# Performance work log

Hardware: AMD Instinct MI355X
Metric: run time of the kernel (lower is better)

The kernel has to match this reference:

```python
import jax, jax.numpy as jnp
import numpy as np

NUM_EMB = 512
EMB_DIM = 64
COMMIT = 0.25
DECAY = 0.99
EPS = 1e-05


def setup_inputs() -> dict:
    key = jax.random.key(0)
    k1, k2, k3 = jax.random.split(key, 3)
    inputs = jax.random.normal(k1, (EMB_DIM, 16, 8192), dtype=jnp.float32)  # [D, B, T]
    embedding = jax.random.normal(k2, (NUM_EMB, EMB_DIM), dtype=jnp.float32)
    ema_w = jax.random.normal(k3, (NUM_EMB, EMB_DIM), dtype=jnp.float32)
    ema_cluster_size = jnp.zeros((NUM_EMB,), dtype=jnp.float32)
    return {"inputs": inputs, "embedding": embedding, "ema_w": ema_w,
            "ema_cluster_size": ema_cluster_size}


def reference(inputs, embedding, ema_w, ema_cluster_size):
    # [D, B, T] -> [B, T, D]
    x = jnp.transpose(inputs, (1, 2, 0))
    in_shape = x.shape
    flat = x.reshape(-1, EMB_DIM)  # [N, D]

    # Squared L2 distances to every codebook entry: [N, K]
    distances = (jnp.sum(flat ** 2, axis=1, keepdims=True)
                 + jnp.sum(embedding ** 2, axis=1)
                 - 2.0 * flat @ embedding.T)
    idx = jnp.argmin(distances, axis=1)                       # [N]
    encodings = jax.nn.one_hot(idx, NUM_EMB, dtype=jnp.float32)  # [N, K]

    # EMA codebook update (training mode). torch wraps results in nn.Parameter,
    # which detaches them, so we stop_gradient the updated embedding.
    cluster = ema_cluster_size * DECAY + (1.0 - DECAY) * jnp.sum(encodings, axis=0)
    n = jnp.sum(cluster)
    cluster = (cluster + EPS) / (n + NUM_EMB * EPS) * n
    dw = jax.ops.segment_sum(flat, idx, num_segments=NUM_EMB)  # == encodings.T @ flat
    new_ema_w = ema_w * DECAY + (1.0 - DECAY) * dw
    new_emb = jax.lax.stop_gradient(new_ema_w / cluster[:, None])  # [K, D]

    # Quantize via gather (equivalent to encodings @ new_emb)
    quantized = new_emb[idx].reshape(in_shape)  # [B, T, D]

    e_latent_loss = jnp.mean((jax.lax.stop_gradient(quantized) - x) ** 2)
    loss = COMMIT * e_latent_loss

    # Straight-through estimator
    quantized_st = x + jax.lax.stop_gradient(quantized - x)

    avg_probs = jnp.mean(encodings, axis=0)
    perplexity = jnp.exp(-jnp.sum(avg_probs * jnp.log(avg_probs + 1e-10)))

    return (loss, jnp.transpose(quantized_st, (2, 0, 1)), perplexity, encodings, distances)
```

## Files before the change

kernel.cpp:

```cpp
#include <hip/hip_runtime.h>

#define NTOT 131072
#define KCB  512
#define DIM  64

__device__ __forceinline__ float wave_sum(float v) {
#pragma unroll
  for (int off = 32; off; off >>= 1) v += __shfl_xor(v, off, 64);
  return v;
}

__global__ __launch_bounds__(512, 1) void k_prep(
    const float* __restrict__ emb, float* __restrict__ embT,
    float* __restrict__ embsq)
{
  const int k = threadIdx.x;
  float sq = 0.f;
#pragma unroll 8
  for (int d = 0; d < DIM; ++d) {
    const float e = emb[k * DIM + d];
    sq = fmaf(e, e, sq);
    embT[d * KCB + k] = -2.f * e;
  }
  embsq[k] = sq;
}

__global__ __launch_bounds__(512, 3) void k_dist(
    const float* __restrict__ x_g,
    const float* __restrict__ embT,
    const float* __restrict__ embsq,
    float* __restrict__ dist_out,
    float* __restrict__ enc_out,
    int* __restrict__ idx_out,
    unsigned* __restrict__ cnt_g,
    float* __restrict__ dw_g)
{
  __shared__ __align__(16) float xls[8][8][65];
  __shared__ unsigned lcnt[KCB];

  const int t = threadIdx.x;
  const int lane = t & 63;
  const int w = t >> 6;

  lcnt[t] = 0u;
  __syncthreads();

  const float4 eb0 = *reinterpret_cast<const float4*>(embsq + 4 * lane);
  const float4 eb1 = *reinterpret_cast<const float4*>(embsq + 256 + 4 * lane);
  float ebr[8] = {eb0.x, eb0.y, eb0.z, eb0.w, eb1.x, eb1.y, eb1.z, eb1.w};

  const int nb = blockIdx.x * 512;
  const int r_own = lane & 7;
  const int dgc   = lane >> 3;

  float xv[8];
  {
    const int n0w = nb + w * 8;
#pragma unroll
    for (int j = 0; j < 8; ++j)
      xv[j] = x_g[(size_t)(dgc * 8 + j) * NTOT + n0w + r_own];
  }

  for (int tt = 0; tt < 8; ++tt) {
    const int n0w = nb + tt * 64 + w * 8;

    asm volatile("" ::: "memory");

#pragma unroll
    for (int j = 0; j < 8; ++j)
      xls[w][r_own][dgc * 8 + j] = xv[j];

    asm volatile("" ::: "memory");

    float ps = 0.f;
#pragma unroll
    for (int j = 0; j < 8; ++j) ps = fmaf(xv[j], xv[j], ps);
    ps += __shfl_xor(ps, 8, 64);
    ps += __shfl_xor(ps, 16, 64);
    ps += __shfl_xor(ps, 32, 64);

    float xr[8];
#pragma unroll
    for (int r = 0; r < 8; ++r) xr[r] = xls[w][r][lane];

    float acc[8][8];
#pragma unroll
    for (int r = 0; r < 8; ++r)
#pragma unroll
      for (int j = 0; j < 8; ++j) acc[r][j] = ebr[j];

#pragma unroll 2
    for (int d = 0; d < DIM; ++d) {
      const float* er = embT + d * KCB + 4 * lane;
      const float4 e0 = *reinterpret_cast<const float4*>(er);
      const float4 e1 = *reinterpret_cast<const float4*>(er + 256);
#pragma unroll
      for (int r = 0; r < 8; ++r) {
        const float s = __uint_as_float(
            __builtin_amdgcn_readlane(__float_as_uint(xr[r]), d));
        acc[r][0] = fmaf(s, e0.x, acc[r][0]);
        acc[r][1] = fmaf(s, e0.y, acc[r][1]);
        acc[r][2] = fmaf(s, e0.z, acc[r][2]);
        acc[r][3] = fmaf(s, e0.w, acc[r][3]);
        acc[r][4] = fmaf(s, e1.x, acc[r][4]);
        acc[r][5] = fmaf(s, e1.y, acc[r][5]);
        acc[r][6] = fmaf(s, e1.z, acc[r][6]);
        acc[r][7] = fmaf(s, e1.w, acc[r][7]);
      }
    }

    if (tt < 7) {
      const int n1w = nb + (tt + 1) * 64 + w * 8;
#pragma unroll
      for (int j = 0; j < 8; ++j)
        xv[j] = x_g[(size_t)(dgc * 8 + j) * NTOT + n1w + r_own];
    }
    asm volatile("" ::: "memory");

#pragma unroll
    for (int r = 0; r < 8; ++r) {
      const int nr = n0w + r;
      const float xs = __uint_as_float(
          __builtin_amdgcn_readlane(__float_as_uint(ps), r));
      float dv[8];
#pragma unroll
      for (int j = 0; j < 8; ++j) dv[j] = acc[r][j] + xs;

      unsigned long long best = ~0ull;
#pragma unroll
      for (int j = 0; j < 8; ++j) {
        const unsigned kk = (j < 4) ? (unsigned)(4 * lane + j)
                                    : (unsigned)(256 + 4 * lane + (j - 4));
        const unsigned long long pk =
            ((unsigned long long)__float_as_uint(dv[j]) << 32) | kk;
        best = pk < best ? pk : best;
      }
#pragma unroll
      for (int off = 32; off; off >>= 1) {
        const unsigned long long o = __shfl_xor(best, off, 64);
        best = o < best ? o : best;
      }
      const int kmin = (int)(best & 0xFFFFFFFFull);

      float* dp = dist_out + (size_t)nr * KCB + 4 * lane;
      float4 q;
      q.x = dv[0]; q.y = dv[1]; q.z = dv[2]; q.w = dv[3];
      *reinterpret_cast<float4*>(dp) = q;
      q.x = dv[4]; q.y = dv[5]; q.z = dv[6]; q.w = dv[7];
      *reinterpret_cast<float4*>(dp + 256) = q;

      float* ep = enc_out + (size_t)nr * KCB + 4 * lane;
      const int k0 = 4 * lane;
      float4 z;
      z.x = (kmin == k0)     ? 1.f : 0.f;
      z.y = (kmin == k0 + 1) ? 1.f : 0.f;
      z.z = (kmin == k0 + 2) ? 1.f : 0.f;
      z.w = (kmin == k0 + 3) ? 1.f : 0.f;
      *reinterpret_cast<float4*>(ep) = z;
      z.x = (kmin == 256 + k0)     ? 1.f : 0.f;
      z.y = (kmin == 256 + k0 + 1) ? 1.f : 0.f;
      z.z = (kmin == 256 + k0 + 2) ? 1.f : 0.f;
      z.w = (kmin == 256 + k0 + 3) ? 1.f : 0.f;
      *reinterpret_cast<float4*>(ep + 256) = z;

      if (lane == 0) {
        idx_out[nr] = kmin;
        atomicAdd(&lcnt[kmin], 1u);
      }
      unsafeAtomicAdd(dw_g + ((size_t)kmin << 6) + lane, xr[r]);
    }
  }

  __syncthreads();
  if (lcnt[t]) atomicAdd(&cnt_g[t], lcnt[t]);
}

__global__ __launch_bounds__(512, 1) void k_final(
    const float* __restrict__ ema_w, const float* __restrict__ ema_cs,
    const unsigned* __restrict__ cnt, const float* __restrict__ dw,
    float* __restrict__ nemb, float* __restrict__ out)
{
  __shared__ float red[8];
  __shared__ float bc;
  const int t = threadIdx.x;
  const int lane = t & 63, w = t >> 6;

  const float c = (float)cnt[t];
  const float craw = ema_cs[t] * 0.99f + 0.01f * c;

  float s = wave_sum(craw);
  if (lane == 0) red[w] = s;
  __syncthreads();
  if (t == 0) {
    float a = 0.f;
#pragma unroll
    for (int i = 0; i < 8; ++i) a += red[i];
    bc = a;
  }
  __syncthreads();
  const float n = bc;
  const float clus = (craw + 1e-5f) / (n + 512.f * 1e-5f) * n;

  const float4* wr = reinterpret_cast<const float4*>(ema_w + t * 64);
  const float4* dr = reinterpret_cast<const float4*>(dw + t * 64);
  float4* nr = reinterpret_cast<float4*>(nemb + t * 64);
#pragma unroll
  for (int q = 0; q < 16; ++q) {
    const float4 wv = wr[q], dv = dr[q];
    float4 o;
    o.x = (wv.x * 0.99f + 0.01f * dv.x) / clus;
    o.y = (wv.y * 0.99f + 0.01f * dv.y) / clus;
    o.z = (wv.z * 0.99f + 0.01f * dv.z) / clus;
    o.w = (wv.w * 0.99f + 0.01f * dv.w) / clus;
    nr[q] = o;
  }

  const float p = c * (1.f / 131072.f);
  const float term = p * logf(p + 1e-10f);
  float s2 = wave_sum(term);
  if (lane == 0) red[w] = s2;
  __syncthreads();
  if (t == 0) {
    float a = 0.f;
#pragma unroll
    for (int i = 0; i < 8; ++i) a += red[i];
    out[8388609] = expf(-a);
  }
}

__global__ __launch_bounds__(256, 4) void k_quant(
    const float* __restrict__ x_g, const int* __restrict__ idx_g,
    const float* __restrict__ nemb, float* __restrict__ out)
{
  float lsum = 0.f;
  const int stride = gridDim.x * 256;
  for (int i = blockIdx.x * 256 + threadIdx.x; i < (DIM * NTOT / 4); i += stride) {
    const int d = i >> 15;
    const int n4 = i & ((NTOT / 4) - 1);
    const float4 xv = *reinterpret_cast<const float4*>(x_g + ((size_t)d << 17) + 4 * n4);
    const int4 id = *reinterpret_cast<const int4*>(idx_g + 4 * n4);
    const float q0 = nemb[(id.x << 6) + d];
    const float q1 = nemb[(id.y << 6) + d];
    const float q2 = nemb[(id.z << 6) + d];
    const float q3 = nemb[(id.w << 6) + d];
    const float e0 = q0 - xv.x, e1 = q1 - xv.y, e2 = q2 - xv.z, e3 = q3 - xv.w;
    float* op = out + 1 + ((size_t)d << 17) + 4 * n4;
    op[0] = xv.x + e0;
    op[1] = xv.y + e1;
    op[2] = xv.z + e2;
    op[3] = xv.w + e3;
    lsum += e0 * e0 + e1 * e1 + e2 * e2 + e3 * e3;
  }
  lsum = wave_sum(lsum);
  __shared__ float wsum[4];
  const int lane = threadIdx.x & 63, w = threadIdx.x >> 6;
  if (lane == 0) wsum[w] = lsum;
  __syncthreads();
  if (threadIdx.x == 0)
    unsafeAtomicAdd(out, (wsum[0] + wsum[1] + wsum[2] + wsum[3]) * (0.25f / 8388608.f));
}

extern "C" void kernel_launch(void* const* d_in, const int* in_sizes, int n_in,
                              void* d_out, int out_size, void* d_ws, size_t ws_size,
                              hipStream_t stream) {
  const float* x      = (const float*)d_in[0];
  const float* emb    = (const float*)d_in[1];
  const float* ema_w  = (const float*)d_in[2];
  const float* ema_cs = (const float*)d_in[3];
  float* out = (float*)d_out;

  float* enc_out  = out + 8388610;
  float* dist_out = out + 75497474;

  char* ws = (char*)d_ws;
  float*    dw    = (float*)ws;
  unsigned* cnt   = (unsigned*)(ws + 131072);
  float*    nemb  = (float*)(ws + 133120);
  int*      idx   = (int*)(ws + 264192);
  float*    embT  = (float*)(ws + 788480);
  float*    embsq = (float*)(ws + 919552);

  hipMemsetAsync(d_ws, 0, 133120, stream);
  hipMemsetAsync(d_out, 0, sizeof(float), stream);

  k_prep<<<1, 512, 0, stream>>>(emb, embT, embsq);
  k_dist<<<256, 512, 0, stream>>>(x, embT, embsq, dist_out, enc_out, idx, cnt, dw);
  k_final<<<1, 512, 0, stream>>>(ema_w, ema_cs, cnt, dw, nemb, out);
  k_quant<<<2048, 256, 0, stream>>>(x, idx, nemb, out);
}
```

Baseline: 274.9 us.

## Stage transposed codebook in LDS and use 1024-thread distance blocks

The distance kernel now loads the codebook directly, scaled by -2 and transposed into a 128KB shared-memory tile, instead of reading a global transposed copy built by the prep kernel. Blocks grow to 1024 threads (16 waves) so each block handles its 512 rows in 4 iterations, and the x staging buffer uses an XOR swizzle in place of padding. Per-block shared-memory count reduction is replaced by direct global atomics. Serving the inner-loop codebook reads from LDS is meant to cut global/L2 traffic, but the large LDS footprint limits occupancy to one block per CU, and the global counter atomics add contention.

```diff
diff --git a/kernel.cpp b/kernel.cpp
--- a/kernel.cpp
+++ b/kernel.cpp
@@ -11,23 +11,23 @@
 }
 
 __global__ __launch_bounds__(512, 1) void k_prep(
-    const float* __restrict__ emb, float* __restrict__ embT,
-    float* __restrict__ embsq)
+    const float* __restrict__ emb, float* __restrict__ embsq)
 {
   const int k = threadIdx.x;
+  const float4* er = reinterpret_cast<const float4*>(emb + k * DIM);
   float sq = 0.f;
-#pragma unroll 8
-  for (int d = 0; d < DIM; ++d) {
-    const float e = emb[k * DIM + d];
-    sq = fmaf(e, e, sq);
-    embT[d * KCB + k] = -2.f * e;
+#pragma unroll
+  for (int q = 0; q < 16; ++q) {
+    const float4 e = er[q];
+    sq = fmaf(e.x, e.x, sq); sq = fmaf(e.y, e.y, sq);
+    sq = fmaf(e.z, e.z, sq); sq = fmaf(e.w, e.w, sq);
   }
   embsq[k] = sq;
 }
 
-__global__ __launch_bounds__(512, 3) void k_dist(
+__global__ __launch_bounds__(1024) void k_dist(
     const float* __restrict__ x_g,
-    const float* __restrict__ embT,
+    const float* __restrict__ emb_g,
     const float* __restrict__ embsq,
     float* __restrict__ dist_out,
     float* __restrict__ enc_out,
@@ -35,19 +35,31 @@
     unsigned* __restrict__ cnt_g,
     float* __restrict__ dw_g)
 {
-  __shared__ __align__(16) float xls[8][8][65];
-  __shared__ unsigned lcnt[KCB];
+  __shared__ __align__(16) float embt[DIM][KCB];
+  __shared__ __align__(16) float xls[16][8][DIM];
 
   const int t = threadIdx.x;
   const int lane = t & 63;
   const int w = t >> 6;
 
-  lcnt[t] = 0u;
+  {
+    const int ke = t & 511;
+    const int dh = (t >> 9) * 32;
+    const float* er = emb_g + ke * DIM + dh;
+#pragma unroll
+    for (int d0 = 0; d0 < 32; d0 += 4) {
+      const float4 e = *reinterpret_cast<const float4*>(er + d0);
+      embt[dh + d0 + 0][ke] = -2.f * e.x;
+      embt[dh + d0 + 1][ke] = -2.f * e.y;
+      embt[dh + d0 + 2][ke] = -2.f * e.z;
+      embt[dh + d0 + 3][ke] = -2.f * e.w;
+    }
+  }
   __syncthreads();
 
   const float4 eb0 = *reinterpret_cast<const float4*>(embsq + 4 * lane);
   const float4 eb1 = *reinterpret_cast<const float4*>(embsq + 256 + 4 * lane);
-  float ebr[8] = {eb0.x, eb0.y, eb0.z, eb0.w, eb1.x, eb1.y, eb1.z, eb1.w};
+  const float ebr[8] = {eb0.x, eb0.y, eb0.z, eb0.w, eb1.x, eb1.y, eb1.z, eb1.w};
 
   const int nb = blockIdx.x * 512;
   const int r_own = lane & 7;
@@ -61,14 +73,14 @@
       xv[j] = x_g[(size_t)(dgc * 8 + j) * NTOT + n0w + r_own];
   }
 
-  for (int tt = 0; tt < 8; ++tt) {
-    const int n0w = nb + tt * 64 + w * 8;
+  for (int tt = 0; tt < 4; ++tt) {
+    const int n0w = nb + tt * 128 + w * 8;
 
     asm volatile("" ::: "memory");
 
 #pragma unroll
     for (int j = 0; j < 8; ++j)
-      xls[w][r_own][dgc * 8 + j] = xv[j];
+      xls[w][r_own][(dgc * 8 + j) ^ r_own] = xv[j];
 
     asm volatile("" ::: "memory");
 
@@ -81,7 +93,7 @@
 
     float xr[8];
 #pragma unroll
-    for (int r = 0; r < 8; ++r) xr[r] = xls[w][r][lane];
+    for (int r = 0; r < 8; ++r) xr[r] = xls[w][r][lane ^ r];
 
     float acc[8][8];
 #pragma unroll
@@ -91,9 +103,8 @@
 
 #pragma unroll 2
     for (int d = 0; d < DIM; ++d) {
-      const float* er = embT + d * KCB + 4 * lane;
-      const float4 e0 = *reinterpret_cast<const float4*>(er);
-      const float4 e1 = *reinterpret_cast<const float4*>(er + 256);
+      const float4 e0 = *reinterpret_cast<const float4*>(&embt[d][4 * lane]);
+      const float4 e1 = *reinterpret_cast<const float4*>(&embt[d][256 + 4 * lane]);
 #pragma unroll
       for (int r = 0; r < 8; ++r) {
         const float s = __uint_as_float(
@@ -109,8 +120,8 @@
       }
     }
 
-    if (tt < 7) {
-      const int n1w = nb + (tt + 1) * 64 + w * 8;
+    if (tt < 3) {
+      const int n1w = nb + (tt + 1) * 128 + w * 8;
 #pragma unroll
       for (int j = 0; j < 8; ++j)
         xv[j] = x_g[(size_t)(dgc * 8 + j) * NTOT + n1w + r_own];
@@ -122,9 +133,8 @@
       const int nr = n0w + r;
       const float xs = __uint_as_float(
           __builtin_amdgcn_readlane(__float_as_uint(ps), r));
-      float dv[8];
-#pragma unroll
-      for (int j = 0; j < 8; ++j) dv[j] = acc[r][j] + xs;
+#pragma unroll
+      for (int j = 0; j < 8; ++j) acc[r][j] += xs;
 
       unsigned long long best = ~0ull;
 #pragma unroll
@@ -132,7 +142,7 @@
         const unsigned kk = (j < 4) ? (unsigned)(4 * lane + j)
                                     : (unsigned)(256 + 4 * lane + (j - 4));
         const unsigned long long pk =
-            ((unsigned long long)__float_as_uint(dv[j]) << 32) | kk;
+            ((unsigned long long)__float_as_uint(acc[r][j]) << 32) | kk;
         best = pk < best ? pk : best;
       }
 #pragma unroll
@@ -144,9 +154,9 @@
 
       float* dp = dist_out + (size_t)nr * KCB + 4 * lane;
       float4 q;
-      q.x = dv[0]; q.y = dv[1]; q.z = dv[2]; q.w = dv[3];
+      q.x = acc[r][0]; q.y = acc[r][1]; q.z = acc[r][2]; q.w = acc[r][3];
       *reinterpret_cast<float4*>(dp) = q;
-      q.x = dv[4]; q.y = dv[5]; q.z = dv[6]; q.w = dv[7];
+      q.x = acc[r][4]; q.y = acc[r][5]; q.z = acc[r][6]; q.w = acc[r][7];
       *reinterpret_cast<float4*>(dp + 256) = q;
 
       float* ep = enc_out + (size_t)nr * KCB + 4 * lane;
@@ -165,14 +175,11 @@
 
       if (lane == 0) {
         idx_out[nr] = kmin;
-        atomicAdd(&lcnt[kmin], 1u);
+        atomicAdd(&cnt_g[kmin], 1u);
       }
       unsafeAtomicAdd(dw_g + ((size_t)kmin << 6) + lane, xr[r]);
     }
   }
-
-  __syncthreads();
-  if (lcnt[t]) atomicAdd(&cnt_g[t], lcnt[t]);
 }
 
 __global__ __launch_bounds__(512, 1) void k_final(
@@ -277,14 +284,13 @@
   unsigned* cnt   = (unsigned*)(ws + 131072);
   float*    nemb  = (float*)(ws + 133120);
   int*      idx   = (int*)(ws + 264192);
-  float*    embT  = (float*)(ws + 788480);
-  float*    embsq = (float*)(ws + 919552);
+  float*    embsq = (float*)(ws + 788480);
 
   hipMemsetAsync(d_ws, 0, 133120, stream);
   hipMemsetAsync(d_out, 0, sizeof(float), stream);
 
-  k_prep<<<1, 512, 0, stream>>>(emb, embT, embsq);
-  k_dist<<<256, 512, 0, stream>>>(x, embT, embsq, dist_out, enc_out, idx, cnt, dw);
+  k_prep<<<1, 512, 0, stream>>>(emb, embsq);
+  k_dist<<<256, 1024, 0, stream>>>(x, emb, embsq, dist_out, enc_out, idx, cnt, dw);
   k_final<<<1, 512, 0, stream>>>(ema_w, ema_cs, cnt, dw, nemb, out);
   k_quant<<<2048, 256, 0, stream>>>(x, idx, nemb, out);
 }
```

Measured after the change: 311.9 us. 1.13x slower.

## Compute distances with split-bf16 MFMA instead of FP32 FMA loops

Applied to the files above, without the earlier changes.

The distance GEMM moves from scalar FP32 FMAs with readlane broadcasts to MFMA 16x16x32 bf16 instructions. Both x and the codebook are split into hi and lo bf16 parts, with three products per pair to approximate FP32 accuracy. Each wave now handles 64 rows at once, with swizzled LDS staging, and counts go straight to global atomics instead of an LDS histogram. The trade-offs are reduced precision that can flip argmin ties, dist stores that are no longer coalesced (scalar strided writes), and a lower occupancy bound.

```diff
diff --git a/kernel.cpp b/kernel.cpp
--- a/kernel.cpp
+++ b/kernel.cpp
@@ -4,6 +4,17 @@
 #define KCB  512
 #define DIM  64
 
+typedef __attribute__((ext_vector_type(8))) short bf16x8;
+typedef __attribute__((ext_vector_type(4))) float f32x4;
+
+__device__ __forceinline__ unsigned short f2bf(float f) {
+  unsigned u = __float_as_uint(f);
+  u = u + 0x7FFFu + ((u >> 16) & 1u);
+  return (unsigned short)(u >> 16);
+}
+__device__ __forceinline__ float bf2f(unsigned short h) {
+  return __uint_as_float(((unsigned)h) << 16);
+}
 __device__ __forceinline__ float wave_sum(float v) {
 #pragma unroll
   for (int off = 32; off; off >>= 1) v += __shfl_xor(v, off, 64);
@@ -11,8 +22,8 @@
 }
 
 __global__ __launch_bounds__(512, 1) void k_prep(
-    const float* __restrict__ emb, float* __restrict__ embT,
-    float* __restrict__ embsq)
+    const float* __restrict__ emb, unsigned short* __restrict__ eh,
+    unsigned short* __restrict__ el, float* __restrict__ embsq)
 {
   const int k = threadIdx.x;
   float sq = 0.f;
@@ -20,14 +31,18 @@
   for (int d = 0; d < DIM; ++d) {
     const float e = emb[k * DIM + d];
     sq = fmaf(e, e, sq);
-    embT[d * KCB + k] = -2.f * e;
+    const float m = -2.f * e;
+    const unsigned short h = f2bf(m);
+    eh[k * DIM + d] = h;
+    el[k * DIM + d] = f2bf(m - bf2f(h));
   }
   embsq[k] = sq;
 }
 
-__global__ __launch_bounds__(512, 3) void k_dist(
+__global__ __launch_bounds__(512, 2) void k_dist(
     const float* __restrict__ x_g,
-    const float* __restrict__ embT,
+    const unsigned short* __restrict__ eh_g,
+    const unsigned short* __restrict__ el_g,
     const float* __restrict__ embsq,
     float* __restrict__ dist_out,
     float* __restrict__ enc_out,
@@ -35,144 +50,160 @@
     unsigned* __restrict__ cnt_g,
     float* __restrict__ dw_g)
 {
-  __shared__ __align__(16) float xls[8][8][65];
-  __shared__ unsigned lcnt[KCB];
+  __shared__ unsigned short xls[8][2][64][64];
+  __shared__ float xsq_l[8][64];
+  __shared__ int   kmin_l[8][64];
 
   const int t = threadIdx.x;
   const int lane = t & 63;
   const int w = t >> 6;
-
-  lcnt[t] = 0u;
-  __syncthreads();
-
-  const float4 eb0 = *reinterpret_cast<const float4*>(embsq + 4 * lane);
-  const float4 eb1 = *reinterpret_cast<const float4*>(embsq + 256 + 4 * lane);
-  float ebr[8] = {eb0.x, eb0.y, eb0.z, eb0.w, eb1.x, eb1.y, eb1.z, eb1.w};
-
-  const int nb = blockIdx.x * 512;
-  const int r_own = lane & 7;
-  const int dgc   = lane >> 3;
-
-  float xv[8];
+  const int n0 = blockIdx.x * 512 + w * 64;
+
   {
-    const int n0w = nb + w * 8;
-#pragma unroll
-    for (int j = 0; j < 8; ++j)
-      xv[j] = x_g[(size_t)(dgc * 8 + j) * NTOT + n0w + r_own];
-  }
-
-  for (int tt = 0; tt < 8; ++tt) {
-    const int n0w = nb + tt * 64 + w * 8;
-
-    asm volatile("" ::: "memory");
-
-#pragma unroll
-    for (int j = 0; j < 8; ++j)
-      xls[w][r_own][dgc * 8 + j] = xv[j];
-
-    asm volatile("" ::: "memory");
-
-    float ps = 0.f;
-#pragma unroll
-    for (int j = 0; j < 8; ++j) ps = fmaf(xv[j], xv[j], ps);
-    ps += __shfl_xor(ps, 8, 64);
-    ps += __shfl_xor(ps, 16, 64);
-    ps += __shfl_xor(ps, 32, 64);
-
-    float xr[8];
-#pragma unroll
-    for (int r = 0; r < 8; ++r) xr[r] = xls[w][r][lane];
-
-    float acc[8][8];
-#pragma unroll
-    for (int r = 0; r < 8; ++r)
-#pragma unroll
-      for (int j = 0; j < 8; ++j) acc[r][j] = ebr[j];
-
-#pragma unroll 2
-    for (int d = 0; d < DIM; ++d) {
-      const float* er = embT + d * KCB + 4 * lane;
-      const float4 e0 = *reinterpret_cast<const float4*>(er);
-      const float4 e1 = *reinterpret_cast<const float4*>(er + 256);
-#pragma unroll
-      for (int r = 0; r < 8; ++r) {
-        const float s = __uint_as_float(
-            __builtin_amdgcn_readlane(__float_as_uint(xr[r]), d));
-        acc[r][0] = fmaf(s, e0.x, acc[r][0]);
-        acc[r][1] = fmaf(s, e0.y, acc[r][1]);
-        acc[r][2] = fmaf(s, e0.z, acc[r][2]);
-        acc[r][3] = fmaf(s, e0.w, acc[r][3]);
-        acc[r][4] = fmaf(s, e1.x, acc[r][4]);
-        acc[r][5] = fmaf(s, e1.y, acc[r][5]);
-        acc[r][6] = fmaf(s, e1.z, acc[r][6]);
-        acc[r][7] = fmaf(s, e1.w, acc[r][7]);
+    float sq = 0.f;
+#pragma unroll
+    for (int half = 0; half < 2; ++half) {
+      float v[32];
+#pragma unroll
+      for (int d = 0; d < 32; ++d)
+        v[d] = x_g[(size_t)(half * 32 + d) * NTOT + n0 + lane];
+#pragma unroll
+      for (int d = 0; d < 32; ++d) {
+        const float f = v[d];
+        sq = fmaf(f, f, sq);
+        const unsigned short h = f2bf(f);
+        const unsigned short lo = f2bf(f - bf2f(h));
+        const int dd = half * 32 + d;
+        const int pos = ((((dd >> 3) ^ (lane & 7)) << 3) | (dd & 7));
+        xls[w][0][lane][pos] = h;
+        xls[w][1][lane][pos] = lo;
       }
     }
-
-    if (tt < 7) {
-      const int n1w = nb + (tt + 1) * 64 + w * 8;
-#pragma unroll
-      for (int j = 0; j < 8; ++j)
-        xv[j] = x_g[(size_t)(dgc * 8 + j) * NTOT + n1w + r_own];
-    }
-    asm volatile("" ::: "memory");
-
-#pragma unroll
-    for (int r = 0; r < 8; ++r) {
-      const int nr = n0w + r;
-      const float xs = __uint_as_float(
-          __builtin_amdgcn_readlane(__float_as_uint(ps), r));
-      float dv[8];
-#pragma unroll
-      for (int j = 0; j < 8; ++j) dv[j] = acc[r][j] + xs;
-
-      unsigned long long best = ~0ull;
-#pragma unroll
-      for (int j = 0; j < 8; ++j) {
-        const unsigned kk = (j < 4) ? (unsigned)(4 * lane + j)
-                                    : (unsigned)(256 + 4 * lane + (j - 4));
-        const unsigned long long pk =
-            ((unsigned long long)__float_as_uint(dv[j]) << 32) | kk;
-        best = pk < best ? pk : best;
+    xsq_l[w][lane] = sq;
+  }
+  asm volatile("" ::: "memory");
+
+  bf16x8 af[4][2][2];
+#pragma unroll
+  for (int rg = 0; rg < 4; ++rg) {
+    const int row = rg * 16 + (lane & 15);
+#pragma unroll
+    for (int ds = 0; ds < 2; ++ds) {
+      const int c = (ds * 4 + (lane >> 4)) ^ (row & 7);
+#pragma unroll
+      for (int hl = 0; hl < 2; ++hl)
+        af[rg][ds][hl] =
+            *reinterpret_cast<const bf16x8*>(&xls[w][hl][row][c << 3]);
+    }
+  }
+
+  float xsq_r[4][4];
+#pragma unroll
+  for (int rg = 0; rg < 4; ++rg)
+#pragma unroll
+    for (int j = 0; j < 4; ++j)
+      xsq_r[rg][j] = xsq_l[w][rg * 16 + (lane >> 4) * 4 + j];
+
+  unsigned long long mn[4][4];
+#pragma unroll
+  for (int rg = 0; rg < 4; ++rg)
+#pragma unroll
+    for (int j = 0; j < 4; ++j) mn[rg][j] = ~0ull;
+
+  for (int kc = 0; kc < 8; ++kc) {
+    const int kbase = kc * 64;
+    f32x4 acc[4][4];
+#pragma unroll
+    for (int rg = 0; rg < 4; ++rg)
+#pragma unroll
+      for (int kg = 0; kg < 4; ++kg) acc[rg][kg] = (f32x4){0.f, 0.f, 0.f, 0.f};
+
+#pragma unroll
+    for (int kg = 0; kg < 4; ++kg) {
+      const int kcode = kbase + kg * 16 + (lane & 15);
+      const unsigned short* ph = eh_g + kcode * 64 + (lane >> 4) * 8;
+      const unsigned short* pl = el_g + kcode * 64 + (lane >> 4) * 8;
+      const bf16x8 beh0 = *reinterpret_cast<const bf16x8*>(ph);
+      const bf16x8 beh1 = *reinterpret_cast<const bf16x8*>(ph + 32);
+      const bf16x8 bel0 = *reinterpret_cast<const bf16x8*>(pl);
+      const bf16x8 bel1 = *reinterpret_cast<const bf16x8*>(pl + 32);
+#pragma unroll
+      for (int rg = 0; rg < 4; ++rg) {
+        f32x4 a = acc[rg][kg];
+        a = __builtin_amdgcn_mfma_f32_16x16x32_bf16(af[rg][0][0], beh0, a, 0, 0, 0);
+        a = __builtin_amdgcn_mfma_f32_16x16x32_bf16(af[rg][0][0], bel0, a, 0, 0, 0);
+        a = __builtin_amdgcn_mfma_f32_16x16x32_bf16(af[rg][0][1], beh0, a, 0, 0, 0);
+        a = __builtin_amdgcn_mfma_f32_16x16x32_bf16(af[rg][1][0], beh1, a, 0, 0, 0);
+        a = __builtin_amdgcn_mfma_f32_16x16x32_bf16(af[rg][1][0], bel1, a, 0, 0, 0);
+        a = __builtin_amdgcn_mfma_f32_16x16x32_bf16(af[rg][1][1], beh1, a, 0, 0, 0);
+        acc[rg][kg] = a;
       }
-#pragma unroll
-      for (int off = 32; off; off >>= 1) {
-        const unsigned long long o = __shfl_xor(best, off, 64);
-        best = o < best ? o : best;
+    }
+
+#pragma unroll
+    for (int kg = 0; kg < 4; ++kg) {
+      const unsigned kk0 = (unsigned)(kbase + kg * 16 + (lane & 15));
+      const float eq = embsq[kk0];
+#pragma unroll
+      for (int rg = 0; rg < 4; ++rg) {
+#pragma unroll
+        for (int j = 0; j < 4; ++j) {
+          const float dist = acc[rg][kg][j] + xsq_r[rg][j] + eq;
+          dist_out[(size_t)(n0 + rg * 16 + (lane >> 4) * 4 + j) * KCB + kk0] = dist;
+          const unsigned long long pk =
+              ((unsigned long long)__float_as_uint(dist) << 32) | kk0;
+          mn[rg][j] = pk < mn[rg][j] ? pk : mn[rg][j];
+        }
       }
-      const int kmin = (int)(best & 0xFFFFFFFFull);
-
-      float* dp = dist_out + (size_t)nr * KCB + 4 * lane;
-      float4 q;
-      q.x = dv[0]; q.y = dv[1]; q.z = dv[2]; q.w = dv[3];
-      *reinterpret_cast<float4*>(dp) = q;
-      q.x = dv[4]; q.y = dv[5]; q.z = dv[6]; q.w = dv[7];
-      *reinterpret_cast<float4*>(dp + 256) = q;
-
-      float* ep = enc_out + (size_t)nr * KCB + 4 * lane;
-      const int k0 = 4 * lane;
-      float4 z;
-      z.x = (kmin == k0)     ? 1.f : 0.f;
-      z.y = (kmin == k0 + 1) ? 1.f : 0.f;
-      z.z = (kmin == k0 + 2) ? 1.f : 0.f;
-      z.w = (kmin == k0 + 3) ? 1.f : 0.f;
-      *reinterpret_cast<float4*>(ep) = z;
-      z.x = (kmin == 256 + k0)     ? 1.f : 0.f;
-      z.y = (kmin == 256 + k0 + 1) ? 1.f : 0.f;
-      z.z = (kmin == 256 + k0 + 2) ? 1.f : 0.f;
-      z.w = (kmin == 256 + k0 + 3) ? 1.f : 0.f;
-      *reinterpret_cast<float4*>(ep + 256) = z;
-
-      if (lane == 0) {
-        idx_out[nr] = kmin;
-        atomicAdd(&lcnt[kmin], 1u);
+    }
+  }
+
+#pragma unroll
+  for (int rg = 0; rg < 4; ++rg)
+#pragma unroll
+    for (int j = 0; j < 4; ++j) {
+#pragma unroll
+      for (int m = 1; m < 16; m <<= 1) {
+        const unsigned long long o = __shfl_xor(mn[rg][j], m, 64);
+        mn[rg][j] = o < mn[rg][j] ? o : mn[rg][j];
       }
-      unsafeAtomicAdd(dw_g + ((size_t)kmin << 6) + lane, xr[r]);
-    }
-  }
-
-  __syncthreads();
-  if (lcnt[t]) atomicAdd(&cnt_g[t], lcnt[t]);
+    }
+  if ((lane & 15) == 0) {
+#pragma unroll
+    for (int rg = 0; rg < 4; ++rg)
+#pragma unroll
+      for (int j = 0; j < 4; ++j)
+        kmin_l[w][rg * 16 + (lane >> 4) * 4 + j] =
+            (int)(mn[rg][j] & 0xFFFFFFFFull);
+  }
+  asm volatile("" ::: "memory");
+
+  {
+    const int km = kmin_l[w][lane];
+    idx_out[n0 + lane] = km;
+    atomicAdd(&cnt_g[km], 1u);
+  }
+
+  for (int r = 0; r < 64; ++r) {
+    const int km = kmin_l[w][r];
+    const int base = lane * 8;
+    float4 z0, z1;
+    z0.x = (km == base)     ? 1.f : 0.f;
+    z0.y = (km == base + 1) ? 1.f : 0.f;
+    z0.z = (km == base + 2) ? 1.f : 0.f;
+    z0.w = (km == base + 3) ? 1.f : 0.f;
+    z1.x = (km == base + 4) ? 1.f : 0.f;
+    z1.y = (km == base + 5) ? 1.f : 0.f;
+    z1.z = (km == base + 6) ? 1.f : 0.f;
+    z1.w = (km == base + 7) ? 1.f : 0.f;
+    float* ep = enc_out + (size_t)(n0 + r) * KCB + base;
+    *reinterpret_cast<float4*>(ep) = z0;
+    *reinterpret_cast<float4*>(ep + 4) = z1;
+
+    const int pos = ((((lane >> 3) ^ (r & 7)) << 3) | (lane & 7));
+    const float xv = bf2f(xls[w][0][r][pos]) + bf2f(xls[w][1][r][pos]);
+    unsafeAtomicAdd(dw_g + ((size_t)km << 6) + lane, xv);
+  }
 }
 
 __global__ __launch_bounds__(512, 1) void k_final(
@@ -273,18 +304,19 @@
   float* dist_out = out + 75497474;
 
   char* ws = (char*)d_ws;
-  float*    dw    = (float*)ws;
-  unsigned* cnt   = (unsigned*)(ws + 131072);
-  float*    nemb  = (float*)(ws + 133120);
-  int*      idx   = (int*)(ws + 264192);
-  float*    embT  = (float*)(ws + 788480);
-  float*    embsq = (float*)(ws + 919552);
+  float*          dw    = (float*)ws;
+  unsigned*       cnt   = (unsigned*)(ws + 131072);
+  float*          nemb  = (float*)(ws + 133120);
+  int*            idx   = (int*)(ws + 264192);
+  float*          embsq = (float*)(ws + 788480);
+  unsigned short* eh    = (unsigned short*)(ws + 790528);
+  unsigned short* el    = (unsigned short*)(ws + 856064);
 
   hipMemsetAsync(d_ws, 0, 133120, stream);
   hipMemsetAsync(d_out, 0, sizeof(float), stream);
 
-  k_prep<<<1, 512, 0, stream>>>(emb, embT, embsq);
-  k_dist<<<256, 512, 0, stream>>>(x, embT, embsq, dist_out, enc_out, idx, cnt, dw);
+  k_prep<<<1, 512, 0, stream>>>(emb, eh, el, embsq);
+  k_dist<<<256, 512, 0, stream>>>(x, eh, el, embsq, dist_out, enc_out, idx, cnt, dw);
   k_final<<<1, 512, 0, stream>>>(ema_w, ema_cs, cnt, dw, nemb, out);
   k_quant<<<2048, 256, 0, stream>>>(x, idx, nemb, out);
 }
```

Result: slower. 347.8 us (+26.6%).
